# Performance work log

Hardware: AMD Instinct MI355X
Metric: run time of the kernel (lower is better)

## Reference

```python
import jax, jax.numpy as jnp
import numpy as np
from jax import lax

LAMBD = 1.0
KAPPA = 0.1
N_ITERS = 400  # fixed unroll count; PGD converges well within this for these scales


def _project_simplex(v):
    # Euclidean projection of each row of v onto {w : w >= 0, sum(w) = 1}.
    n = v.shape[-1]
    u = -jnp.sort(-v, axis=-1)                       # descending sort
    css = jnp.cumsum(u, axis=-1)
    j = jnp.arange(1, n + 1, dtype=v.dtype)
    cond = u + (1.0 - css) / j > 0                   # monotone condition; rho = #True
    rho = jnp.sum(cond, axis=-1, keepdims=True)      # [B,1], always >= 1
    css_rho = jnp.take_along_axis(css, rho - 1, axis=-1)
    tau = (css_rho - 1.0) / rho.astype(v.dtype)
    return jnp.maximum(v - tau, 0.0)


def _solve_robust_mvo(mu, U, A):
    # min_w -mu'w + kappa*||A w||_2 + (lambd/2)*||U w||_2^2  s.t. w in simplex
    B, n = mu.shape
    G1 = jnp.einsum('bij,bik->bjk', U, U)            # U^T U, [B,n,n]
    G2 = jnp.einsum('bij,bik->bjk', A, A)            # A^T A, [B,n,n]
    # Lipschitz upper bound via Frobenius norms -> safe fixed step size
    froU2 = jnp.sum(U * U, axis=(-2, -1), keepdims=False)[:, None]   # ||U||_F^2, [B,1]
    froA = jnp.sqrt(jnp.sum(A * A, axis=(-2, -1)))[:, None]          # ||A||_F,   [B,1]
    step = 1.0 / (LAMBD * froU2 + KAPPA * froA + 1.0)

    w0 = jnp.full((B, n), 1.0 / n, dtype=mu.dtype)

    def body(w, _):
        g1w = jnp.einsum('bij,bj->bi', G1, w)        # U^T U w
        g2w = jnp.einsum('bij,bj->bi', G2, w)        # A^T A w
        nrm = jnp.sqrt(jnp.maximum(jnp.sum(w * g2w, axis=-1, keepdims=True), 1e-12))
        grad = -mu + LAMBD * g1w + KAPPA * g2w / nrm
        w_new = _project_simplex(w - step * grad)
        return w_new, None

    w, _ = lax.scan(body, w0, None, length=N_ITERS)
    # mirror the torch post-processing: clamp + renormalize
    w = jnp.maximum(w, 0.0)
    return w / (jnp.sum(w, axis=-1, keepdims=True) + 1e-12)


def setup_inputs() -> dict:
    key = jax.random.key(0)
    k1, k2, k3 = jax.random.split(key, 3)
    B, n = 512, 256
    mu = jax.random.normal(k1, (B, n), dtype=jnp.float32)
    U = jax.random.normal(k2, (B, n, n), dtype=jnp.float32)
    A = jax.random.normal(k3, (B, n, n), dtype=jnp.float32)
    return {"mu": mu, "U": U, "A": A}


def reference(mu, U, A):
    return _solve_robust_mvo(mu, U, A)
```

## Files before the change

### kernel.cpp

```cpp
#include <hip/hip_runtime.h>
#include <math.h>

#define NB 512
#define NN 256
#define N_ITERS 400
#define KAPPA_F 0.1f

typedef _Float16 half2_t __attribute__((ext_vector_type(2)));
typedef _Float16 half8_t __attribute__((ext_vector_type(8)));

__device__ inline float fdot2f(half2_t a, half2_t b, float c) {
#if __has_builtin(__builtin_amdgcn_fdot2)
  return __builtin_amdgcn_fdot2(a, b, c, false);
#else
  return (float)a.x * (float)b.x + (float)a.y * (float)b.y + c;
#endif
}


#define SB() __builtin_amdgcn_sched_barrier(0);
#define PAIR(V, K) __builtin_shufflevector(V, V, 2*(K), 2*(K)+1)

#define ZA(J) cA##J.x=0.f; cA##J.y=0.f; cA##J.z=0.f; cA##J.w=0.f;
#define GMAC(J, F) { cA##J.x = fmaf(a0, F.x, cA##J.x); cA##J.y = fmaf(a0, F.y, cA##J.y); \
                     cA##J.z = fmaf(a0, F.z, cA##J.z); cA##J.w = fmaf(a0, F.w, cA##J.w); }
#define GRAM1(SRC, RB, DOFRO) do { \
  const float4* __restrict__ src4 = (const float4*)(SRC); \
  ZA(0) ZA(1) ZA(2) ZA(3) ZA(4) ZA(5) ZA(6) ZA(7) \
  float4 st = src4[t]; \
  _Pragma("unroll 1") \
  for (int kt = 0; kt < 32; ++kt) { \
    __syncthreads(); \
    ((float4*)As)[t] = st; \
    if (DOFRO) fro += st.x*st.x + st.y*st.y + st.z*st.z + st.w*st.w; \
    __syncthreads(); \
    if (kt < 31) st = src4[(kt + 1) * 512 + t]; \
    _Pragma("unroll 1") \
    for (int k = 0; k < 8; ++k) { \
      const float* rowp = As + k * NN; \
      float a0 = rowp[(RB) + lane]; \
      const float4* rp4 = (const float4*)(rowp + 32 * wv); \
      { float4 f0=rp4[0], f1=rp4[1], f2=rp4[2], f3=rp4[3]; \
        GMAC(0,f0) GMAC(1,f1) GMAC(2,f2) GMAC(3,f3) } \
      { float4 f0=rp4[4], f1=rp4[5], f2=rp4[6], f3=rp4[7]; \
        GMAC(4,f0) GMAC(5,f1) GMAC(6,f2) GMAC(7,f3) } \
    } \
  } \
} while (0)

#define CV1(P, GA, GB, J) { \
  float x0=cA##J.x, x1=cA##J.y, x2=cA##J.z, x3=cA##J.w; \
  const int cb = 32*wv + 4*(J); \
  if (cb+0==row_) { diag1[row_]=x0; x0=0.f; } \
  if (cb+1==row_) { diag1[row_]=x1; x1=0.f; } \
  if (cb+2==row_) { diag1[row_]=x2; x2=0.f; } \
  if (cb+3==row_) { diag1[row_]=x3; x3=0.f; } \
  { half2_t h; h.x=(_Float16)x0; h.y=(_Float16)x1; g##P##GA = h; \
    h.x=(_Float16)x2; h.y=(_Float16)x3; g##P##GB = h; } }
#define CVTG1(P, RB) { const int row_ = (RB) + lane; \
  CV1(P,0,1,0) CV1(P,2,3,1) CV1(P,4,5,2) CV1(P,6,7,3) \
  CV1(P,8,9,4) CV1(P,10,11,5) CV1(P,12,13,6) CV1(P,14,15,7) }

#define PK2(CJ, CK, M) { \
  float x0=cA##CJ.x, x1=cA##CJ.y, x2=cA##CJ.z, x3=cA##CJ.w; \
  float x4=cA##CK.x, x5=cA##CK.y, x6=cA##CK.z, x7=cA##CK.w; \
  const int cb = 32*wv + 8*(M); \
  if (cb+0==row_) { diag2[row_]=x0; x0=0.f; } \
  if (cb+1==row_) { diag2[row_]=x1; x1=0.f; } \
  if (cb+2==row_) { diag2[row_]=x2; x2=0.f; } \
  if (cb+3==row_) { diag2[row_]=x3; x3=0.f; } \
  if (cb+4==row_) { diag2[row_]=x4; x4=0.f; } \
  if (cb+5==row_) { diag2[row_]=x5; x5=0.f; } \
  if (cb+6==row_) { diag2[row_]=x6; x6=0.f; } \
  if (cb+7==row_) { diag2[row_]=x7; x7=0.f; } \
  half8_t h8; \
  h8[0]=(_Float16)x0; h8[1]=(_Float16)x1; h8[2]=(_Float16)x2; h8[3]=(_Float16)x3; \
  h8[4]=(_Float16)x4; h8[5]=(_Float16)x5; h8[6]=(_Float16)x6; h8[7]=(_Float16)x7; \
  *(half8_t*)((char*)g2s + row_*512 + ((((cb>>3) ^ (row_&31)))<<4)) = h8; }
#define PACKG2(RB) { const int row_ = (RB) + lane; \
  PK2(0,1,0) PK2(2,3,1) PK2(4,5,2) PK2(6,7,3) }

#define LH(I, SA, SBo, R) { \
  R##0 = *(const half8_t*)(g2b + (SA) + (I)*32768); \
  R##1 = *(const half8_t*)(g2b + (SBo) + (I)*32768); }

#define D2H(I, R) { \
  p2##I = fdot2f(PAIR(R##0,0), PAIR(uh0,0), p2##I); \
  p2##I = fdot2f(PAIR(R##0,1), PAIR(uh0,1), p2##I); \
  p2##I = fdot2f(PAIR(R##0,2), PAIR(uh0,2), p2##I); \
  p2##I = fdot2f(PAIR(R##0,3), PAIR(uh0,3), p2##I); \
  p2##I = fdot2f(PAIR(R##1,0), PAIR(uh1,0), p2##I); \
  p2##I = fdot2f(PAIR(R##1,1), PAIR(uh1,1), p2##I); \
  p2##I = fdot2f(PAIR(R##1,2), PAIR(uh1,2), p2##I); \
  p2##I = fdot2f(PAIR(R##1,3), PAIR(uh1,3), p2##I); }

#define G1H0(P, I) { \
  p1##I = fdot2f(g##P##0, PAIR(uh0,0), p1##I); \
  p1##I = fdot2f(g##P##1, PAIR(uh0,1), p1##I); \
  p1##I = fdot2f(g##P##2, PAIR(uh0,2), p1##I); \
  p1##I = fdot2f(g##P##3, PAIR(uh0,3), p1##I); \
  p1##I = fdot2f(g##P##4, PAIR(uh1,0), p1##I); \
  p1##I = fdot2f(g##P##5, PAIR(uh1,1), p1##I); \
  p1##I = fdot2f(g##P##6, PAIR(uh1,2), p1##I); \
  p1##I = fdot2f(g##P##7, PAIR(uh1,3), p1##I); }
#define G1H1(P, I) { \
  p1##I = fdot2f(g##P##8,  PAIR(uh0,0), p1##I); \
  p1##I = fdot2f(g##P##9,  PAIR(uh0,1), p1##I); \
  p1##I = fdot2f(g##P##10, PAIR(uh0,2), p1##I); \
  p1##I = fdot2f(g##P##11, PAIR(uh0,3), p1##I); \
  p1##I = fdot2f(g##P##12, PAIR(uh1,0), p1##I); \
  p1##I = fdot2f(g##P##13, PAIR(uh1,1), p1##I); \
  p1##I = fdot2f(g##P##14, PAIR(uh1,2), p1##I); \
  p1##I = fdot2f(g##P##15, PAIR(uh1,3), p1##I); }

#define COMB(I) { \
  const int rr = 64 * (I) + lane; \
  float2 x0 = parts[rr],          x1 = parts[NN + rr]; \
  float2 x2 = parts[2*NN + rr],   x3 = parts[3*NN + rr]; \
  float2 x4 = parts[4*NN + rr],   x5 = parts[5*NN + rr]; \
  float2 x6 = parts[6*NN + rr],   x7 = parts[7*NN + rr]; \
  q1##I = ((x0.x+x1.x)+(x2.x+x3.x))+((x4.x+x5.x)+(x6.x+x7.x)); \
  q2##I = ((x0.y+x1.y)+(x2.y+x3.y))+((x4.y+x5.y)+(x6.y+x7.y)); }

__global__
__attribute__((amdgpu_flat_work_group_size(512, 512)))
__attribute__((amdgpu_waves_per_eu(2, 2)))
void mvo_kernel(const float* __restrict__ mu,
                const float* __restrict__ U,
                const float* __restrict__ A,
                float* __restrict__ out)
{
  __shared__ alignas(16) _Float16 g2s[NN * NN];
  __shared__ alignas(16) float2 parts[8 * NN];
  __shared__ alignas(16) float    wsf[NN];
  __shared__ alignas(16) _Float16 whs[NN];
  __shared__ float mus[NN];
  __shared__ float diag1[NN];
  __shared__ float diag2[NN];
  __shared__ float dslot[8];
  __shared__ float slotA[8];
  __shared__ float slotB[8];
  __shared__ int   doneflag;

  float* As = (float*)parts;

  const int t    = threadIdx.x;
  const int b    = blockIdx.x;
  const int lane = t & 63;
  const int wv   = t >> 6;

  const float* __restrict__ Ub = U + (size_t)b * NN * NN;
  const float* __restrict__ Ab = A + (size_t)b * NN * NN;

  if (t == 0) doneflag = 0;
  if (t < NN) mus[t] = mu[b * NN + t];

  half2_t gA0,gA1,gA2,gA3,gA4,gA5,gA6,gA7,gA8,gA9,gA10,gA11,gA12,gA13,gA14,gA15;
  half2_t gB0,gB1,gB2,gB3,gB4,gB5,gB6,gB7,gB8,gB9,gB10,gB11,gB12,gB13,gB14,gB15;
  half2_t gC0,gC1,gC2,gC3,gC4,gC5,gC6,gC7,gC8,gC9,gC10,gC11,gC12,gC13,gC14,gC15;
  half2_t gD0,gD1,gD2,gD3,gD4,gD5,gD6,gD7,gD8,gD9,gD10,gD11,gD12,gD13,gD14,gD15;
  float4 cA0, cA1, cA2, cA3, cA4, cA5, cA6, cA7;
  float fro, d1, d2;

  fro = 0.f;
  GRAM1(Ab, 0, 1);   PACKG2(0);
  GRAM1(Ab, 64, 0);  PACKG2(64);
  GRAM1(Ab, 128, 0); PACKG2(128);
  GRAM1(Ab, 192, 0); PACKG2(192);
  d2 = fro;
  fro = 0.f;
  GRAM1(Ub, 0, 1);   CVTG1(A, 0);
  GRAM1(Ub, 64, 0);  CVTG1(B, 64);
  GRAM1(Ub, 128, 0); CVTG1(C, 128);
  GRAM1(Ub, 192, 0); CVTG1(D, 192);
  d1 = fro;

  #pragma unroll
  for (int m = 1; m < 64; m <<= 1) {
    d1 += __shfl_xor(d1, m, 64);
    d2 += __shfl_xor(d2, m, 64);
  }
  if (lane == 0) { slotA[wv] = d1; slotB[wv] = d2; }
  if (t < NN) { wsf[t] = 1.0f / 256.0f; whs[t] = (_Float16)(1.0f / 256.0f); }
  __syncthreads();
  float froU2 = 0.f, froA2 = 0.f;
  #pragma unroll
  for (int k = 0; k < 8; ++k) { froU2 += slotA[k]; froA2 += slotB[k]; }
  const float step = 1.0f / (froU2 + KAPPA_F * sqrtf(froA2) + 1.0f);

  const char* g2b = (const char*)g2s + lane * 512;
  const int l31 = lane & 31;
  const int sc0 = ((4*wv + 0) ^ l31) << 4;
  const int sc1 = ((4*wv + 1) ^ l31) << 4;
  const int sc2 = ((4*wv + 2) ^ l31) << 4;
  const int sc3 = ((4*wv + 3) ^ l31) << 4;
  const half8_t* whp = (const half8_t*)whs + 4 * wv;
  const int dsel = lane >> 5;

  #pragma unroll 1
  for (int it = 0; it < N_ITERS; ++it) {
    float p10=0.f, p11=0.f, p12=0.f, p13=0.f;
    float p20=0.f, p21=0.f, p22=0.f, p23=0.f;
    {
      half8_t uh0 = whp[0], uh1 = whp[1];
      half8_t A0, A1, B0, B1;
      LH(0, sc0, sc1, A)
      LH(1, sc0, sc1, B)
      G1H0(A, 0) G1H0(B, 1) G1H0(C, 2) G1H0(D, 3)
      D2H(0, A) SB() LH(2, sc0, sc1, A)
      D2H(1, B) SB() LH(3, sc0, sc1, B)
      D2H(2, A) SB()
      D2H(3, B) SB()
    }
    {
      half8_t uh0 = whp[2], uh1 = whp[3];
      half8_t A0, A1, B0, B1;
      LH(0, sc2, sc3, A)
      LH(1, sc2, sc3, B)
      G1H1(A, 0) G1H1(B, 1) G1H1(C, 2) G1H1(D, 3)
      D2H(0, A) SB() LH(2, sc2, sc3, A)
      D2H(1, B) SB() LH(3, sc2, sc3, B)
      D2H(2, A) SB()
      D2H(3, B) SB()
    }
    float w_r0 = wsf[lane],       w_r1 = wsf[64 + lane];
    float w_r2 = wsf[128 + lane], w_r3 = wsf[192 + lane];
    if (wv == dsel)     { p10 = fmaf(diag1[lane],     w_r0, p10);
                          p20 = fmaf(diag2[lane],     w_r0, p20); }
    if (wv == 2 + dsel) { p11 = fmaf(diag1[64+lane],  w_r1, p11);
                          p21 = fmaf(diag2[64+lane],  w_r1, p21); }
    if (wv == 4 + dsel) { p12 = fmaf(diag1[128+lane], w_r2, p12);
                          p22 = fmaf(diag2[128+lane], w_r2, p22); }
    if (wv == 6 + dsel) { p13 = fmaf(diag1[192+lane], w_r3, p13);
                          p23 = fmaf(diag2[192+lane], w_r3, p23); }
    float dpart = fmaf(p20, w_r0, fmaf(p21, w_r1, fmaf(p22, w_r2, p23 * w_r3)));
    #pragma unroll
    for (int m = 1; m < 64; m <<= 1) dpart += __shfl_xor(dpart, m, 64);
    parts[wv * NN + lane]       = make_float2(p10, p20);
    parts[wv * NN + 64 + lane]  = make_float2(p11, p21);
    parts[wv * NN + 128 + lane] = make_float2(p12, p22);
    parts[wv * NN + 192 + lane] = make_float2(p13, p23);
    if (lane == 0) dslot[wv] = dpart;
    __syncthreads();

    if (wv == 0) {
      float q10, q11, q12, q13, q20, q21, q22, q23;
      COMB(0) COMB(1) COMB(2) COMB(3)
      float dot = ((dslot[0]+dslot[1])+(dslot[2]+dslot[3]))
                + ((dslot[4]+dslot[5])+(dslot[6]+dslot[7]));
      float nrm = sqrtf(fmaxf(dot, 1e-12f));
      float kon = KAPPA_F / nrm;
      float v0 = w_r0 - step * (q10 + kon * q20 - mus[lane]);
      float v1 = w_r1 - step * (q11 + kon * q21 - mus[64 + lane]);
      float v2 = w_r2 - step * (q12 + kon * q22 - mus[128 + lane]);
      float v3 = w_r3 - step * (q13 + kon * q23 - mus[192 + lane]);
      float s = v0 + v1 + v2 + v3;
      #pragma unroll
      for (int m = 1; m < 64; m <<= 1) s += __shfl_xor(s, m, 64);
      float tau = (s - 1.0f) * (1.0f / 256.0f);
      float cprev = 256.0f;
      for (int ms = 0; ms < 24; ++ms) {
        float s2 = (v0 > tau ? v0 : 0.f) + (v1 > tau ? v1 : 0.f)
                 + (v2 > tau ? v2 : 0.f) + (v3 > tau ? v3 : 0.f);
        float c2 = (v0 > tau ? 1.f : 0.f) + (v1 > tau ? 1.f : 0.f)
                 + (v2 > tau ? 1.f : 0.f) + (v3 > tau ? 1.f : 0.f);
        #pragma unroll
        for (int m = 1; m < 64; m <<= 1) {
          s2 += __shfl_xor(s2, m, 64);
          c2 += __shfl_xor(c2, m, 64);
        }
        if (c2 == cprev) break;
        tau = (s2 - 1.0f) / c2;
        cprev = c2;
      }
      float nw0 = fmaxf(v0 - tau, 0.f);
      float nw1 = fmaxf(v1 - tau, 0.f);
      float nw2 = fmaxf(v2 - tau, 0.f);
      float nw3 = fmaxf(v3 - tau, 0.f);
      int same = (nw0 == w_r0) && (nw1 == w_r1) && (nw2 == w_r2) && (nw3 == w_r3);
      int conv = __all(same);
      wsf[lane]       = nw0; wsf[64 + lane]  = nw1;
      wsf[128 + lane] = nw2; wsf[192 + lane] = nw3;
      whs[lane]       = (_Float16)nw0; whs[64 + lane]  = (_Float16)nw1;
      whs[128 + lane] = (_Float16)nw2; whs[192 + lane] = (_Float16)nw3;
      if (lane == 0) doneflag = conv;
    }
    __syncthreads();
    if (doneflag) break;
  }

  if (wv == 0) {
    float w_0 = wsf[lane],       w_1 = wsf[64 + lane];
    float w_2 = wsf[128 + lane], w_3 = wsf[192 + lane];
    float s = w_0 + w_1 + w_2 + w_3;
    #pragma unroll
    for (int m = 1; m < 64; m <<= 1) s += __shfl_xor(s, m, 64);
    float inv = 1.0f / (s + 1e-12f);
    float* ob = out + b * NN;
    ob[lane]        = w_0 * inv;
    ob[64 + lane]   = w_1 * inv;
    ob[128 + lane]  = w_2 * inv;
    ob[192 + lane]  = w_3 * inv;
  }
}

extern "C" void kernel_launch(void* const* d_in, const int* in_sizes, int n_in,
                              void* d_out, int out_size, void* d_ws, size_t ws_size,
                              hipStream_t stream) {
  const float* mu = (const float*)d_in[0];
  const float* U  = (const float*)d_in[1];
  const float* A  = (const float*)d_in[2];
  float* out = (float*)d_out;
  hipLaunchKernelGGL(mvo_kernel, dim3(NB), dim3(512), 0, stream, mu, U, A, out);
}
```

Baseline: 2.662 ms.

## Keep both Gram matrices register-resident and compute Gram blocks two row-groups at a time

Stores the fp16 A^T A Gram slice in registers alongside U^T U instead of in a swizzled 128KB LDS buffer, so each PGD iteration's matvec reads no Gram data from LDS. The Gram construction is restructured to compute two 64-row blocks per pass over the input, halving the number of global sweeps and barriers. This doubles the register footprint for Gram storage and accumulators, raising spill risk at 512 threads with waves_per_eu 2, and drops the manual sched_barrier scheduling.

```diff
diff --git a/kernel.cpp b/kernel.cpp
--- a/kernel.cpp
+++ b/kernel.cpp
@@ -18,100 +18,74 @@
 }
 
 
-#define SB() __builtin_amdgcn_sched_barrier(0);
 #define PAIR(V, K) __builtin_shufflevector(V, V, 2*(K), 2*(K)+1)
 
-#define ZA(J) cA##J.x=0.f; cA##J.y=0.f; cA##J.z=0.f; cA##J.w=0.f;
-#define GMAC(J, F) { cA##J.x = fmaf(a0, F.x, cA##J.x); cA##J.y = fmaf(a0, F.y, cA##J.y); \
-                     cA##J.z = fmaf(a0, F.z, cA##J.z); cA##J.w = fmaf(a0, F.w, cA##J.w); }
-#define GRAM1(SRC, RB, DOFRO) do { \
+#define DOT8(ACC, R, UH) \
+  ACC = fdot2f(PAIR(R,0), PAIR(UH,0), ACC); \
+  ACC = fdot2f(PAIR(R,1), PAIR(UH,1), ACC); \
+  ACC = fdot2f(PAIR(R,2), PAIR(UH,2), ACC); \
+  ACC = fdot2f(PAIR(R,3), PAIR(UH,3), ACC);
+
+#define ZC(P,J) c##P##J.x=0.f; c##P##J.y=0.f; c##P##J.z=0.f; c##P##J.w=0.f;
+#define ZALL() ZC(A,0) ZC(A,1) ZC(A,2) ZC(A,3) ZC(A,4) ZC(A,5) ZC(A,6) ZC(A,7) \
+               ZC(B,0) ZC(B,1) ZC(B,2) ZC(B,3) ZC(B,4) ZC(B,5) ZC(B,6) ZC(B,7)
+
+#define GMA(J,F) { cA##J.x=fmaf(a0,F.x,cA##J.x); cA##J.y=fmaf(a0,F.y,cA##J.y); \
+                   cA##J.z=fmaf(a0,F.z,cA##J.z); cA##J.w=fmaf(a0,F.w,cA##J.w); }
+#define GMB(J,F) { cB##J.x=fmaf(a1,F.x,cB##J.x); cB##J.y=fmaf(a1,F.y,cB##J.y); \
+                   cB##J.z=fmaf(a1,F.z,cB##J.z); cB##J.w=fmaf(a1,F.w,cB##J.w); }
+
+#define GRAM2(SRC, RB, DOFRO) do { \
   const float4* __restrict__ src4 = (const float4*)(SRC); \
-  ZA(0) ZA(1) ZA(2) ZA(3) ZA(4) ZA(5) ZA(6) ZA(7) \
-  float4 st = src4[t]; \
+  ZALL() \
+  float4 st0 = src4[t], st1 = src4[512 + t]; \
   _Pragma("unroll 1") \
-  for (int kt = 0; kt < 32; ++kt) { \
+  for (int kt = 0; kt < 16; ++kt) { \
     __syncthreads(); \
-    ((float4*)As)[t] = st; \
-    if (DOFRO) fro += st.x*st.x + st.y*st.y + st.z*st.z + st.w*st.w; \
+    ((float4*)As)[t] = st0; \
+    ((float4*)As)[512 + t] = st1; \
+    if (DOFRO) { fro += st0.x*st0.x + st0.y*st0.y + st0.z*st0.z + st0.w*st0.w; \
+                 fro += st1.x*st1.x + st1.y*st1.y + st1.z*st1.z + st1.w*st1.w; } \
     __syncthreads(); \
-    if (kt < 31) st = src4[(kt + 1) * 512 + t]; \
+    if (kt < 15) { st0 = src4[(kt+1)*1024 + t]; st1 = src4[(kt+1)*1024 + 512 + t]; } \
     _Pragma("unroll 1") \
-    for (int k = 0; k < 8; ++k) { \
+    for (int k = 0; k < 16; ++k) { \
       const float* rowp = As + k * NN; \
       float a0 = rowp[(RB) + lane]; \
+      float a1 = rowp[(RB) + 64 + lane]; \
       const float4* rp4 = (const float4*)(rowp + 32 * wv); \
       { float4 f0=rp4[0], f1=rp4[1], f2=rp4[2], f3=rp4[3]; \
-        GMAC(0,f0) GMAC(1,f1) GMAC(2,f2) GMAC(3,f3) } \
-      { float4 f0=rp4[4], f1=rp4[5], f2=rp4[6], f3=rp4[7]; \
-        GMAC(4,f0) GMAC(5,f1) GMAC(6,f2) GMAC(7,f3) } \
+        GMA(0,f0) GMA(1,f1) GMA(2,f2) GMA(3,f3) \
+        GMB(0,f0) GMB(1,f1) GMB(2,f2) GMB(3,f3) } \
+      { float4 f4=rp4[4], f5=rp4[5], f6=rp4[6], f7=rp4[7]; \
+        GMA(4,f4) GMA(5,f5) GMA(6,f6) GMA(7,f7) \
+        GMB(4,f4) GMB(5,f5) GMB(6,f6) GMB(7,f7) } \
     } \
   } \
 } while (0)
 
-#define CV1(P, GA, GB, J) { \
-  float x0=cA##J.x, x1=cA##J.y, x2=cA##J.z, x3=cA##J.w; \
-  const int cb = 32*wv + 4*(J); \
-  if (cb+0==row_) { diag1[row_]=x0; x0=0.f; } \
-  if (cb+1==row_) { diag1[row_]=x1; x1=0.f; } \
-  if (cb+2==row_) { diag1[row_]=x2; x2=0.f; } \
-  if (cb+3==row_) { diag1[row_]=x3; x3=0.f; } \
-  { half2_t h; h.x=(_Float16)x0; h.y=(_Float16)x1; g##P##GA = h; \
-    h.x=(_Float16)x2; h.y=(_Float16)x3; g##P##GB = h; } }
-#define CVTG1(P, RB) { const int row_ = (RB) + lane; \
-  CV1(P,0,1,0) CV1(P,2,3,1) CV1(P,4,5,2) CV1(P,6,7,3) \
-  CV1(P,8,9,4) CV1(P,10,11,5) CV1(P,12,13,6) CV1(P,14,15,7) }
-
-#define PK2(CJ, CK, M) { \
-  float x0=cA##CJ.x, x1=cA##CJ.y, x2=cA##CJ.z, x3=cA##CJ.w; \
-  float x4=cA##CK.x, x5=cA##CK.y, x6=cA##CK.z, x7=cA##CK.w; \
+#define PACK8(RREG, M, DIAG, FA, FB) { \
+  float x0=FA.x, x1=FA.y, x2=FA.z, x3=FA.w; \
+  float x4=FB.x, x5=FB.y, x6=FB.z, x7=FB.w; \
   const int cb = 32*wv + 8*(M); \
-  if (cb+0==row_) { diag2[row_]=x0; x0=0.f; } \
-  if (cb+1==row_) { diag2[row_]=x1; x1=0.f; } \
-  if (cb+2==row_) { diag2[row_]=x2; x2=0.f; } \
-  if (cb+3==row_) { diag2[row_]=x3; x3=0.f; } \
-  if (cb+4==row_) { diag2[row_]=x4; x4=0.f; } \
-  if (cb+5==row_) { diag2[row_]=x5; x5=0.f; } \
-  if (cb+6==row_) { diag2[row_]=x6; x6=0.f; } \
-  if (cb+7==row_) { diag2[row_]=x7; x7=0.f; } \
+  if (cb+0==row_) { DIAG[row_]=x0; x0=0.f; } \
+  if (cb+1==row_) { DIAG[row_]=x1; x1=0.f; } \
+  if (cb+2==row_) { DIAG[row_]=x2; x2=0.f; } \
+  if (cb+3==row_) { DIAG[row_]=x3; x3=0.f; } \
+  if (cb+4==row_) { DIAG[row_]=x4; x4=0.f; } \
+  if (cb+5==row_) { DIAG[row_]=x5; x5=0.f; } \
+  if (cb+6==row_) { DIAG[row_]=x6; x6=0.f; } \
+  if (cb+7==row_) { DIAG[row_]=x7; x7=0.f; } \
   half8_t h8; \
   h8[0]=(_Float16)x0; h8[1]=(_Float16)x1; h8[2]=(_Float16)x2; h8[3]=(_Float16)x3; \
   h8[4]=(_Float16)x4; h8[5]=(_Float16)x5; h8[6]=(_Float16)x6; h8[7]=(_Float16)x7; \
-  *(half8_t*)((char*)g2s + row_*512 + ((((cb>>3) ^ (row_&31)))<<4)) = h8; }
-#define PACKG2(RB) { const int row_ = (RB) + lane; \
-  PK2(0,1,0) PK2(2,3,1) PK2(4,5,2) PK2(6,7,3) }
-
-#define LH(I, SA, SBo, R) { \
-  R##0 = *(const half8_t*)(g2b + (SA) + (I)*32768); \
-  R##1 = *(const half8_t*)(g2b + (SBo) + (I)*32768); }
-
-#define D2H(I, R) { \
-  p2##I = fdot2f(PAIR(R##0,0), PAIR(uh0,0), p2##I); \
-  p2##I = fdot2f(PAIR(R##0,1), PAIR(uh0,1), p2##I); \
-  p2##I = fdot2f(PAIR(R##0,2), PAIR(uh0,2), p2##I); \
-  p2##I = fdot2f(PAIR(R##0,3), PAIR(uh0,3), p2##I); \
-  p2##I = fdot2f(PAIR(R##1,0), PAIR(uh1,0), p2##I); \
-  p2##I = fdot2f(PAIR(R##1,1), PAIR(uh1,1), p2##I); \
-  p2##I = fdot2f(PAIR(R##1,2), PAIR(uh1,2), p2##I); \
-  p2##I = fdot2f(PAIR(R##1,3), PAIR(uh1,3), p2##I); }
-
-#define G1H0(P, I) { \
-  p1##I = fdot2f(g##P##0, PAIR(uh0,0), p1##I); \
-  p1##I = fdot2f(g##P##1, PAIR(uh0,1), p1##I); \
-  p1##I = fdot2f(g##P##2, PAIR(uh0,2), p1##I); \
-  p1##I = fdot2f(g##P##3, PAIR(uh0,3), p1##I); \
-  p1##I = fdot2f(g##P##4, PAIR(uh1,0), p1##I); \
-  p1##I = fdot2f(g##P##5, PAIR(uh1,1), p1##I); \
-  p1##I = fdot2f(g##P##6, PAIR(uh1,2), p1##I); \
-  p1##I = fdot2f(g##P##7, PAIR(uh1,3), p1##I); }
-#define G1H1(P, I) { \
-  p1##I = fdot2f(g##P##8,  PAIR(uh0,0), p1##I); \
-  p1##I = fdot2f(g##P##9,  PAIR(uh0,1), p1##I); \
-  p1##I = fdot2f(g##P##10, PAIR(uh0,2), p1##I); \
-  p1##I = fdot2f(g##P##11, PAIR(uh0,3), p1##I); \
-  p1##I = fdot2f(g##P##12, PAIR(uh1,0), p1##I); \
-  p1##I = fdot2f(g##P##13, PAIR(uh1,1), p1##I); \
-  p1##I = fdot2f(g##P##14, PAIR(uh1,2), p1##I); \
-  p1##I = fdot2f(g##P##15, PAIR(uh1,3), p1##I); }
+  RREG = h8; }
+
+#define PACKG(PFX, CP, DIAG, RB) { const int row_ = (RB) + lane; \
+  PACK8(PFX##0, 0, DIAG, c##CP##0, c##CP##1) \
+  PACK8(PFX##1, 1, DIAG, c##CP##2, c##CP##3) \
+  PACK8(PFX##2, 2, DIAG, c##CP##4, c##CP##5) \
+  PACK8(PFX##3, 3, DIAG, c##CP##6, c##CP##7) }
 
 #define COMB(I) { \
   const int rr = 64 * (I) + lane; \
@@ -130,7 +104,6 @@
                 const float* __restrict__ A,
                 float* __restrict__ out)
 {
-  __shared__ alignas(16) _Float16 g2s[NN * NN];
   __shared__ alignas(16) float2 parts[8 * NN];
   __shared__ alignas(16) float    wsf[NN];
   __shared__ alignas(16) _Float16 whs[NN];
@@ -155,24 +128,23 @@
   if (t == 0) doneflag = 0;
   if (t < NN) mus[t] = mu[b * NN + t];
 
-  half2_t gA0,gA1,gA2,gA3,gA4,gA5,gA6,gA7,gA8,gA9,gA10,gA11,gA12,gA13,gA14,gA15;
-  half2_t gB0,gB1,gB2,gB3,gB4,gB5,gB6,gB7,gB8,gB9,gB10,gB11,gB12,gB13,gB14,gB15;
-  half2_t gC0,gC1,gC2,gC3,gC4,gC5,gC6,gC7,gC8,gC9,gC10,gC11,gC12,gC13,gC14,gC15;
-  half2_t gD0,gD1,gD2,gD3,gD4,gD5,gD6,gD7,gD8,gD9,gD10,gD11,gD12,gD13,gD14,gD15;
-  float4 cA0, cA1, cA2, cA3, cA4, cA5, cA6, cA7;
+  half8_t eA0,eA1,eA2,eA3, eB0,eB1,eB2,eB3, eC0,eC1,eC2,eC3, eD0,eD1,eD2,eD3;
+  half8_t hA0,hA1,hA2,hA3, hB0,hB1,hB2,hB3, hC0,hC1,hC2,hC3, hD0,hD1,hD2,hD3;
+  float4 cA0,cA1,cA2,cA3,cA4,cA5,cA6,cA7;
+  float4 cB0,cB1,cB2,cB3,cB4,cB5,cB6,cB7;
   float fro, d1, d2;
 
   fro = 0.f;
-  GRAM1(Ab, 0, 1);   PACKG2(0);
-  GRAM1(Ab, 64, 0);  PACKG2(64);
-  GRAM1(Ab, 128, 0); PACKG2(128);
-  GRAM1(Ab, 192, 0); PACKG2(192);
+  GRAM2(Ab, 0, 1);
+  PACKG(hA, A, diag2, 0) PACKG(hB, B, diag2, 64)
+  GRAM2(Ab, 128, 0);
+  PACKG(hC, A, diag2, 128) PACKG(hD, B, diag2, 192)
   d2 = fro;
   fro = 0.f;
-  GRAM1(Ub, 0, 1);   CVTG1(A, 0);
-  GRAM1(Ub, 64, 0);  CVTG1(B, 64);
-  GRAM1(Ub, 128, 0); CVTG1(C, 128);
-  GRAM1(Ub, 192, 0); CVTG1(D, 192);
+  GRAM2(Ub, 0, 1);
+  PACKG(eA, A, diag1, 0) PACKG(eB, B, diag1, 64)
+  GRAM2(Ub, 128, 0);
+  PACKG(eC, A, diag1, 128) PACKG(eD, B, diag1, 192)
   d1 = fro;
 
   #pragma unroll
@@ -188,41 +160,23 @@
   for (int k = 0; k < 8; ++k) { froU2 += slotA[k]; froA2 += slotB[k]; }
   const float step = 1.0f / (froU2 + KAPPA_F * sqrtf(froA2) + 1.0f);
 
-  const char* g2b = (const char*)g2s + lane * 512;
-  const int l31 = lane & 31;
-  const int sc0 = ((4*wv + 0) ^ l31) << 4;
-  const int sc1 = ((4*wv + 1) ^ l31) << 4;
-  const int sc2 = ((4*wv + 2) ^ l31) << 4;
-  const int sc3 = ((4*wv + 3) ^ l31) << 4;
   const half8_t* whp = (const half8_t*)whs + 4 * wv;
   const int dsel = lane >> 5;
 
   #pragma unroll 1
   for (int it = 0; it < N_ITERS; ++it) {
+    half8_t uh0 = whp[0], uh1 = whp[1], uh2 = whp[2], uh3 = whp[3];
     float p10=0.f, p11=0.f, p12=0.f, p13=0.f;
     float p20=0.f, p21=0.f, p22=0.f, p23=0.f;
-    {
-      half8_t uh0 = whp[0], uh1 = whp[1];
-      half8_t A0, A1, B0, B1;
-      LH(0, sc0, sc1, A)
-      LH(1, sc0, sc1, B)
-      G1H0(A, 0) G1H0(B, 1) G1H0(C, 2) G1H0(D, 3)
-      D2H(0, A) SB() LH(2, sc0, sc1, A)
-      D2H(1, B) SB() LH(3, sc0, sc1, B)
-      D2H(2, A) SB()
-      D2H(3, B) SB()
-    }
-    {
-      half8_t uh0 = whp[2], uh1 = whp[3];
-      half8_t A0, A1, B0, B1;
-      LH(0, sc2, sc3, A)
-      LH(1, sc2, sc3, B)
-      G1H1(A, 0) G1H1(B, 1) G1H1(C, 2) G1H1(D, 3)
-      D2H(0, A) SB() LH(2, sc2, sc3, A)
-      D2H(1, B) SB() LH(3, sc2, sc3, B)
-      D2H(2, A) SB()
-      D2H(3, B) SB()
-    }
+    DOT8(p10, eA0, uh0) DOT8(p10, eA1, uh1) DOT8(p10, eA2, uh2) DOT8(p10, eA3, uh3)
+    DOT8(p11, eB0, uh0) DOT8(p11, eB1, uh1) DOT8(p11, eB2, uh2) DOT8(p11, eB3, uh3)
+    DOT8(p12, eC0, uh0) DOT8(p12, eC1, uh1) DOT8(p12, eC2, uh2) DOT8(p12, eC3, uh3)
+    DOT8(p13, eD0, uh0) DOT8(p13, eD1, uh1) DOT8(p13, eD2, uh2) DOT8(p13, eD3, uh3)
+    DOT8(p20, hA0, uh0) DOT8(p20, hA1, uh1) DOT8(p20, hA2, uh2) DOT8(p20, hA3, uh3)
+    DOT8(p21, hB0, uh0) DOT8(p21, hB1, uh1) DOT8(p21, hB2, uh2) DOT8(p21, hB3, uh3)
+    DOT8(p22, hC0, uh0) DOT8(p22, hC1, uh1) DOT8(p22, hC2, uh2) DOT8(p22, hC3, uh3)
+    DOT8(p23, hD0, uh0) DOT8(p23, hD1, uh1) DOT8(p23, hD2, uh2) DOT8(p23, hD3, uh3)
+
     float w_r0 = wsf[lane],       w_r1 = wsf[64 + lane];
     float w_r2 = wsf[128 + lane], w_r3 = wsf[192 + lane];
     if (wv == dsel)     { p10 = fmaf(diag1[lane],     w_r0, p10);
```

New measurement: 2.419 ms. 9.1% less time.
